# Kernel optimization log

Measured on AMD Instinct MI355X. Metric: run time of the kernel, lower is better.

## Reference

```python
import jax, jax.numpy as jnp
import numpy as np

BS, LATENT, HID, MAXLEN = 128, 512, 1024, 512

def setup_inputs() -> dict:
    key = jax.random.key(0)
    ks = jax.random.split(key, 12)
    s = 1.0 / np.sqrt(HID)  # pytorch default LSTM init scale
    inp = {}
    inp["decoder_input"] = jax.random.normal(ks[0], (BS, LATENT), jnp.float32)
    inp["lengths"] = jax.random.randint(ks[1], (BS,), 0, MAXLEN)
    # bidirectional single-layer LSTM params (gate order i,f,g,o; combined bias = b_ih+b_hh)
    inp["Wih_f"] = jax.random.uniform(ks[2], (4 * HID, LATENT), jnp.float32, -s, s)
    inp["Whh_f"] = jax.random.uniform(ks[3], (4 * HID, HID), jnp.float32, -s, s)
    inp["b_f"] = jax.random.uniform(ks[4], (4 * HID,), jnp.float32, -s, s)
    inp["Wih_b"] = jax.random.uniform(ks[5], (4 * HID, LATENT), jnp.float32, -s, s)
    inp["Whh_b"] = jax.random.uniform(ks[6], (4 * HID, HID), jnp.float32, -s, s)
    inp["b_b"] = jax.random.uniform(ks[7], (4 * HID,), jnp.float32, -s, s)
    # out: Linear(hidden -> latent); fc1: Linear(2*hidden -> 1)
    inp["W_out"] = jax.random.uniform(ks[8], (LATENT, HID), jnp.float32, -s, s)
    inp["b_out"] = jax.random.uniform(ks[9], (LATENT,), jnp.float32, -s, s)
    inp["W_fc1"] = jax.random.uniform(ks[10], (1, 2 * HID), jnp.float32, -s, s)
    inp["b_fc1"] = jax.random.uniform(ks[11], (1,), jnp.float32, -s, s)
    return inp

def _lstm_cell(x, h, c, Wih, Whh, b):
    z = x @ Wih.T + h @ Whh.T + b  # (bs, 4H)
    i, f, g, o = jnp.split(z, 4, axis=-1)
    c2 = jax.nn.sigmoid(f) * c + jax.nn.sigmoid(i) * jnp.tanh(g)
    h2 = jax.nn.sigmoid(o) * jnp.tanh(c2)
    return h2, c2

def reference(decoder_input, lengths, Wih_f, Whh_f, b_f, Wih_b, Whh_b, b_b,
              W_out, b_out, W_fc1, b_fc1):
    max_len = int(jnp.max(lengths))  # static decode length
    bs = decoder_input.shape[0]
    h0 = jnp.zeros((bs, HID), decoder_input.dtype)

    def step(carry, _):
        x, hf, cf, hb, cb = carry
        # bidirectional LSTM over a length-1 sequence = two cells on same input
        hf, cf = _lstm_cell(x, hf, cf, Wih_f, Whh_f, b_f)
        hb, cb = _lstm_cell(x, hb, cb, Wih_b, Whh_b, b_b)
        out_t = jnp.concatenate([hf, hb], axis=-1)  # (bs, 2H)
        # next input = out(h_n[-1]) i.e. backward-direction hidden
        x_next = hb @ W_out.T + b_out
        return (x_next, hf, cf, hb, cb), out_t

    carry0 = (decoder_input, h0, h0, h0, h0)
    _, outs = jax.lax.scan(step, carry0, xs=None, length=max_len)  # (T, bs, 2H)
    x = jnp.transpose(outs, (1, 0, 2))  # (bs, T, 2H)
    x = jax.nn.relu(x)
    return x @ W_fc1.T + b_fc1  # (bs, T, 1)
```

## Files before the change

kernel.cpp:

```cpp
#include <hip/hip_runtime.h>
#include <math.h>

typedef unsigned short u16;
typedef __attribute__((ext_vector_type(8))) short short8;
typedef __attribute__((ext_vector_type(4))) float f32x4;

__device__ __forceinline__ float sigm(float x) { return 1.0f / (1.0f + expf(-x)); }

__device__ __forceinline__ u16 f2bf(float x) {
    union { float f; unsigned u; } v; v.f = x;
    unsigned r = v.u + 0x7fffu + ((v.u >> 16) & 1u);
    return (u16)(r >> 16);
}
__device__ __forceinline__ float bf2f(u16 h) {
    union { unsigned u; float f; } v; v.u = ((unsigned)h) << 16;
    return v.f;
}
__device__ __forceinline__ f32x4 mfma16(short8 a, short8 b, f32x4 c) {
    return __builtin_amdgcn_mfma_f32_16x16x32_bf16(a, b, c, 0, 0, 0);
}
__device__ __forceinline__ void gl_lds16(const void* g, void* l) {
    __builtin_amdgcn_global_load_lds(
        (const __attribute__((address_space(1))) unsigned int*)g,
        (__attribute__((address_space(3))) unsigned int*)l, 16, 0, 0);
}
__device__ __forceinline__ int swz(int c) { return (c ^ (c >> 2)) & 3; }

#define FENCE() asm volatile("" ::: "memory")

#define STAGE_W(kk, buf)                                                      \
    do {                                                                      \
        gl_lds16(Wsrc + sA + (kk), sm + (buf) * 8192 + lds0);                 \
        gl_lds16(Wsrc + sB + (kk), sm + (buf) * 8192 + lds1);                 \
    } while (0)

#define LOAD_A(kk, AH_, AL_)                                                  \
    do {                                                                      \
        _Pragma("unroll") for (int ks_ = 0; ks_ < 2; ++ks_) {                 \
            AH_[ks_] = *(const short8*)(Ah + aoff + (kk) + ks_ * 32);         \
            AL_[ks_] = *(const short8*)(Al + aoff + (kk) + ks_ * 32);         \
        }                                                                     \
    } while (0)

#define COMPUTE(bix, AH_, AL_, cix)                                           \
    do {                                                                      \
        const char* bb_ = sm + (bix) * 8192;                                  \
        _Pragma("unroll") for (int ks_ = 0; ks_ < 2; ++ks_) {                 \
            short8 bh_[2], bl_[2];                                            \
            _Pragma("unroll") for (int nt_ = 0; nt_ < 2; ++nt_) {             \
                const int col_ = nt_ * 16 + l15;                              \
                const int off_ = ks_ * 2048 + col_ * 64 + ((quad ^ swz(col_)) * 16); \
                bh_[nt_] = *(const short8*)(bb_ + off_);                      \
                bl_[nt_] = *(const short8*)(bb_ + 4096 + off_);               \
            }                                                                 \
            _Pragma("unroll") for (int nt_ = 0; nt_ < 2; ++nt_) {             \
                acc[nt_] = mfma16(AH_[ks_], bh_[nt_], acc[nt_]);              \
                acc[nt_] = mfma16(AL_[ks_], bh_[nt_], acc[nt_]);              \
                acc[nt_] = mfma16(AH_[ks_], bl_[nt_], acc[nt_]);              \
            }                                                                 \
        }                                                                     \
        if (fc1w) {                                                           \
            const int kb_ = koff + (cix) * 64 + quad * 8;                     \
            _Pragma("unroll") for (int ks_ = 0; ks_ < 2; ++ks_) {             \
                const float* wp_ = smWf + kb_ + ks_ * 32;                     \
                const f32x4 w0_ = *(const f32x4*)(wp_);                       \
                const f32x4 w1_ = *(const f32x4*)(wp_ + 4);                   \
                const short8 hv_ = AH_[ks_];                                  \
                const short8 lv_ = AL_[ks_];                                  \
                _Pragma("unroll") for (int e_ = 0; e_ < 8; ++e_) {            \
                    const float v_ = bf2f((u16)hv_[e_]) + bf2f((u16)lv_[e_]); \
                    const float wv_ = (e_ < 4) ? w0_[e_] : w1_[e_ - 4];       \
                    fsum = fmaf(fmaxf(v_, 0.0f), wv_, fsum);                  \
                }                                                             \
            }                                                                 \
        }                                                                     \
    } while (0)

#define ITER(cc, BC, BS, AHU, ALU, AHL, ALL)                                  \
    do {                                                                      \
        asm volatile("s_waitcnt vmcnt(16)" ::: "memory");                     \
        __builtin_amdgcn_s_barrier();                                         \
        FENCE();                                                              \
        STAGE_W(((cc) + 3) * 64, BS);                                         \
        FENCE();                                                              \
        LOAD_A(((cc) + 3) * 64, AHL, ALL);                                    \
        COMPUTE(BC, AHU, ALU, (cc));                                          \
    } while (0)

__global__ __launch_bounds__(256, 2) void k_step(
    const u16* __restrict__ Ah, const u16* __restrict__ Al,
    u16* __restrict__ NAh, u16* __restrict__ NAl,
    const u16* __restrict__ WH, const u16* __restrict__ WL, int wstride,
    int koff_f, int nch_f, int koff_b, int nch_b,
    const float* __restrict__ BR, float* __restrict__ CF, float* __restrict__ CB,
    const float* __restrict__ Wfc1, const float* __restrict__ bfc1,
    float* __restrict__ out, int T, int t)
{
    __shared__ __align__(16) char sm[32768];
    __shared__ __align__(16) char ze[9216];
    __shared__ __align__(16) float smWf[2048];

    const int tid = threadIdx.x, bid = blockIdx.x;
    const int w = tid >> 6, lane = tid & 63, l15 = lane & 15, quad = lane >> 4;
    const int dir = bid >> 8;
    const int rest = bid & 255;
    const int rowhalf = rest >> 7, colgrp = rest & 127;
    const int nbase = dir * 4096 + colgrp * 32;
    const int koff = dir ? koff_b : koff_f;
    const int nch  = dir ? nch_b : nch_f;
    const int r0 = rowhalf * 64 + w * 16;

    const bool fc1b = (dir == 1) && (colgrp == 0);
    const bool fc1w = fc1b && (t > 0);

    const int sp = w >> 1, skh = w & 1;
    const u16* Wsrc = sp ? WL : WH;
    size_t sA, sB;
    int lds0, lds1;
    {
        const int colA = 0 * 16 + (lane >> 2);
        const int colB = 1 * 16 + (lane >> 2);
        const int sa = (lane & 3) ^ swz(colA);
        const int sb = (lane & 3) ^ swz(colB);
        sA = (size_t)(nbase + colA) * wstride + (size_t)(koff + skh * 32 + sa * 8);
        sB = (size_t)(nbase + colB) * wstride + (size_t)(koff + skh * 32 + sb * 8);
        lds0 = sp * 4096 + skh * 2048;
        lds1 = lds0 + 1024;
    }

    const size_t aoff = (size_t)(r0 + l15) * 2048 + (size_t)(koff + quad * 8);

    f32x4 acc[2] = {};
    short8 ah0[2], al0[2], ah1[2], al1[2];
    short8 ah2[2], al2[2], ah3[2], al3[2];
    float fsum = 0.0f;

    if (fc1b) {
        const f32x4 w0 = *(const f32x4*)(Wfc1 + tid * 8);
        const f32x4 w1 = *(const f32x4*)(Wfc1 + tid * 8 + 4);
        *(f32x4*)(smWf + tid * 8) = w0;
        *(f32x4*)(smWf + tid * 8 + 4) = w1;
    }
    asm volatile("s_waitcnt vmcnt(0) lgkmcnt(0)" ::: "memory");

    STAGE_W(0, 0);   FENCE(); LOAD_A(0, ah0, al0);   FENCE();
    STAGE_W(64, 1);  FENCE(); LOAD_A(64, ah1, al1);  FENCE();
    STAGE_W(128, 2); FENCE(); LOAD_A(128, ah2, al2); FENCE();

    for (int c = 0; c < nch; c += 4) {
        ITER(c + 0, 0, 3, ah0, al0, ah3, al3);
        ITER(c + 1, 1, 0, ah1, al1, ah0, al0);
        ITER(c + 2, 2, 1, ah2, al2, ah1, al1);
        ITER(c + 3, 3, 2, ah3, al3, ah2, al2);
    }
    asm volatile("s_waitcnt vmcnt(0)" ::: "memory");

    if (fc1w) {
        const size_t af = (size_t)(r0 + l15) * 2048 + (size_t)(quad * 8);
        for (int c2 = 0; c2 < 16; ++c2) {
#pragma unroll
            for (int ks = 0; ks < 2; ++ks) {
                const int ko = c2 * 64 + ks * 32;
                const short8 hv = *(const short8*)(Ah + af + ko);
                const short8 lv = *(const short8*)(Al + af + ko);
                const float* wp = smWf + ko + quad * 8;
                const f32x4 w0 = *(const f32x4*)(wp);
                const f32x4 w1 = *(const f32x4*)(wp + 4);
#pragma unroll
                for (int e = 0; e < 8; ++e) {
                    const float v = bf2f((u16)hv[e]) + bf2f((u16)lv[e]);
                    const float wv = (e < 4) ? w0[e] : w1[e - 4];
                    fsum = fmaf(fmaxf(v, 0.0f), wv, fsum);
                }
            }
        }
        float v = fsum;
        v += __shfl_xor(v, 16);
        v += __shfl_xor(v, 32);
        if (lane < 16)
            out[(size_t)(r0 + l15) * T + (t - 1)] = v + bfc1[0];
    }

    char* zb = ze + w * 2304;
#pragma unroll
    for (int nt = 0; nt < 2; ++nt)
#pragma unroll
        for (int r = 0; r < 4; ++r)
            *(float*)(zb + (quad * 4 + r) * 144 + (nt * 16 + l15) * 4) = acc[nt][r];

    float* C = dir ? CB : CF;
    const int ul = lane & 7;
#pragma unroll
    for (int p2 = 0; p2 < 2; ++p2) {
        const int ml = p2 * 8 + (lane >> 3);
        const f32x4 z = *(const f32x4*)(zb + ml * 144 + ul * 16);
        const f32x4 b4 = *(const f32x4*)(BR + nbase + ul * 4);
        const float zi = z[0] + b4[0], zf = z[1] + b4[1];
        const float zg = z[2] + b4[2], zo = z[3] + b4[3];
        const int u = colgrp * 8 + ul;
        const int m = r0 + ml;
        const size_t cidx = (size_t)m * 1024 + u;
        const float cold = C[cidx];
        const float c2 = sigm(zf) * cold + sigm(zi) * tanhf(zg);
        const float h2 = sigm(zo) * tanhf(c2);
        C[cidx] = c2;
        const size_t hidx = (size_t)m * 2048 + dir * 1024 + u;
        const u16 hh = f2bf(h2);
        NAh[hidx] = hh;
        NAl[hidx] = f2bf(h2 - bf2f(hh));
    }
}

__global__ __launch_bounds__(256) void k_tail(
    const u16* __restrict__ Ah, const u16* __restrict__ Al,
    const float* __restrict__ Wfc1, const float* __restrict__ bfc1,
    float* __restrict__ out, int T)
{
    __shared__ float red[256];
    const int m = blockIdx.x, tid = threadIdx.x;
    const size_t base = (size_t)m * 2048 + tid * 8;
    const short8 hv = *(const short8*)(Ah + base);
    const short8 lv = *(const short8*)(Al + base);
    float s = 0.0f;
#pragma unroll
    for (int e = 0; e < 8; ++e) {
        const float v = bf2f((u16)hv[e]) + bf2f((u16)lv[e]);
        s = fmaf(fmaxf(v, 0.0f), Wfc1[tid * 8 + e], s);
    }
    red[tid] = s;
    __syncthreads();
    for (int off = 128; off > 0; off >>= 1) {
        if (tid < off) red[tid] += red[tid + off];
        __syncthreads();
    }
    if (tid == 0) out[(size_t)m * T + T - 1] = red[0] + bfc1[0];
}

__global__ __launch_bounds__(256, 1) void k_fold(
    const u16* __restrict__ AH, const u16* __restrict__ AL,
    const u16* __restrict__ BH, const u16* __restrict__ BL,
    const float* __restrict__ Whh_b,
    u16* __restrict__ WH, u16* __restrict__ WL)
{
    const int tid = threadIdx.x, bid = blockIdx.x;
    const int w = tid >> 6, lane = tid & 63, l15 = lane & 15, quad = lane >> 4;
    const int bm = bid >> 4, bn = bid & 15;
    const int ar0 = bm * 64 + (w & 1) * 32;
    const int br0 = bn * 64 + (w >> 1) * 32;
    f32x4 acc[2][2] = {};
    for (int k0 = 0; k0 < 512; k0 += 32) {
        short8 a_h[2], a_l[2], b_h[2], b_l[2];
#pragma unroll
        for (int mt = 0; mt < 2; ++mt) {
            const size_t o = (size_t)(ar0 + mt * 16 + l15) * 512 + k0 + quad * 8;
            a_h[mt] = *(const short8*)(AH + o);
            a_l[mt] = *(const short8*)(AL + o);
        }
#pragma unroll
        for (int nt = 0; nt < 2; ++nt) {
            const size_t o = (size_t)(br0 + nt * 16 + l15) * 512 + k0 + quad * 8;
            b_h[nt] = *(const short8*)(BH + o);
            b_l[nt] = *(const short8*)(BL + o);
        }
#pragma unroll
        for (int mt = 0; mt < 2; ++mt)
#pragma unroll
            for (int nt = 0; nt < 2; ++nt) {
                acc[mt][nt] = mfma16(a_h[mt], b_h[nt], acc[mt][nt]);
                acc[mt][nt] = mfma16(a_l[mt], b_h[nt], acc[mt][nt]);
                acc[mt][nt] = mfma16(a_h[mt], b_l[nt], acc[mt][nt]);
            }
    }
#pragma unroll
    for (int mt = 0; mt < 2; ++mt)
#pragma unroll
        for (int nt = 0; nt < 2; ++nt)
#pragma unroll
            for (int r = 0; r < 4; ++r) {
                const int row = ar0 + mt * 16 + quad * 4 + r;
                const int j = br0 + nt * 16 + l15;
                float v = acc[mt][nt][r];
                if (row >= 4096)
                    v += Whh_b[(size_t)((row & 3) * 1024 + ((row & 4095) >> 2)) * 1024 + j];
                const size_t d = (size_t)row * 2048 + 1024 + j;
                const u16 hh = f2bf(v);
                WH[d] = hh;
                WL[d] = f2bf(v - bf2f(hh));
            }
}

__global__ __launch_bounds__(256) void k_prep(
    const float* __restrict__ dec,
    const float* __restrict__ Wih_f, const float* __restrict__ Whh_f,
    const float* __restrict__ b_f, const float* __restrict__ Wih_b,
    const float* __restrict__ b_b, const float* __restrict__ W_out,
    const float* __restrict__ b_out, const float* __restrict__ b_fc1,
    u16* __restrict__ WihH, u16* __restrict__ WihL,
    u16* __restrict__ WoTH, u16* __restrict__ WoTL,
    float* __restrict__ BR0, float* __restrict__ BR1,
    u16* __restrict__ A0h, u16* __restrict__ A0l,
    u16* __restrict__ WH, u16* __restrict__ WL,
    float* __restrict__ out, int out_size)
{
    const int t = blockIdx.x * 256 + threadIdx.x;
    if (t < 524288) {
        const int colp = t >> 6, kb = (t & 63) * 8;
        const int dir = colp >> 12, u = (colp & 4095) >> 2, g = colp & 3;
        const float* src = (dir ? Wih_b : Wih_f) + (size_t)(g * 1024 + u) * 512 + kb;
        const size_t d = (size_t)colp * 512 + kb;
#pragma unroll
        for (int j = 0; j < 8; ++j) {
            const float v = src[j];
            const u16 hh = f2bf(v);
            WihH[d + j] = hh; WihL[d + j] = f2bf(v - bf2f(hh));
        }
    } else if (t < 589824) {
        const int i = t - 524288, jc = i >> 6, lb = (i & 63) * 8;
#pragma unroll
        for (int jj = 0; jj < 8; ++jj) {
            const float v = W_out[(size_t)(lb + jj) * 1024 + jc];
            const size_t d = (size_t)jc * 512 + lb + jj;
            const u16 hh = f2bf(v);
            WoTH[d] = hh; WoTL[d] = f2bf(v - bf2f(hh));
        }
    } else if (t < 598016) {
        const int colp = t - 589824;
        const int dir = colp >> 12, u = (colp & 4095) >> 2, g = colp & 3;
        const float* Wih = dir ? Wih_b : Wih_f;
        const float s = (dir ? b_b : b_f)[g * 1024 + u];
        BR0[colp] = s;
        float dot = 0.0f;
        for (int l = 0; l < 512; ++l)
            dot += Wih[(size_t)(g * 1024 + u) * 512 + l] * b_out[l];
        BR1[colp] = s + dot;
    } else if (t < 606208) {
        const int i = t - 598016, m = i >> 6, kb = (i & 63) * 8;
#pragma unroll
        for (int j = 0; j < 8; ++j) {
            const float v = dec[(size_t)m * 512 + kb + j];
            const size_t d = (size_t)m * 2048 + kb + j;
            const u16 hh = f2bf(v);
            A0h[d] = hh; A0l[d] = f2bf(v - bf2f(hh));
        }
    } else if (t < 614400) {
        const int base = (t - 606208) * 8;
        const float b0 = b_fc1[0];
#pragma unroll
        for (int j = 0; j < 8; ++j)
            if (base + j < out_size) out[base + j] = b0;
    } else {
        const int i = t - 614400, colp = i >> 7, kb = (i & 127) * 8;
        const int u = colp >> 2, g = colp & 3;
        const float* src = Whh_f + (size_t)(g * 1024 + u) * 1024 + kb;
        const size_t d = (size_t)colp * 2048 + kb;
#pragma unroll
        for (int j = 0; j < 8; ++j) {
            const float v = src[j];
            const u16 hh = f2bf(v);
            WH[d + j] = hh; WL[d + j] = f2bf(v - bf2f(hh));
        }
    }
}

extern "C" void kernel_launch(void* const* d_in, const int* in_sizes, int n_in,
                              void* d_out, int out_size, void* d_ws, size_t ws_size,
                              hipStream_t stream) {
    const float* dec   = (const float*)d_in[0];
    const float* Wih_f = (const float*)d_in[2];
    const float* Whh_f = (const float*)d_in[3];
    const float* b_f   = (const float*)d_in[4];
    const float* Wih_b = (const float*)d_in[5];
    const float* Whh_b = (const float*)d_in[6];
    const float* b_b   = (const float*)d_in[7];
    const float* W_out = (const float*)d_in[8];
    const float* b_out = (const float*)d_in[9];
    const float* W_fc1 = (const float*)d_in[10];
    const float* b_fc1 = (const float*)d_in[11];
    float* out = (float*)d_out;

    char* ws = (char*)d_ws;
    u16* WH    = (u16*)(ws);
    u16* WL    = (u16*)(ws + 33554432);
    u16* WihH  = (u16*)(ws + 67108864);
    u16* WihL  = (u16*)(ws + 75497472);
    u16* WoTH  = (u16*)(ws + 83886080);
    u16* WoTL  = (u16*)(ws + 84934656);
    u16* A0h   = (u16*)(ws + 85983232);
    u16* A0l   = (u16*)(ws + 86507520);
    u16* A1h   = (u16*)(ws + 87031808);
    u16* A1l   = (u16*)(ws + 87556096);
    float* CF  = (float*)(ws + 88080384);
    float* CB  = (float*)(ws + 88604672);
    float* BR0 = (float*)(ws + 89128960);
    float* BR1 = (float*)(ws + 89161728);

    k_prep<<<4448, 256, 0, stream>>>(dec, Wih_f, Whh_f, b_f, Wih_b, b_b,
                                     W_out, b_out, b_fc1,
                                     WihH, WihL, WoTH, WoTL, BR0, BR1,
                                     A0h, A0l, WH, WL, out, out_size);
    k_fold<<<2048, 256, 0, stream>>>(WihH, WihL, WoTH, WoTL, Whh_b, WH, WL);
    hipMemsetAsync(CF, 0, 1048576, stream);

    const int T = out_size / 128;
    u16* Abh[2] = {A0h, A1h};
    u16* Abl[2] = {A0l, A1l};
    for (int t = 0; t < T; ++t) {
        const int in = t & 1, nx = in ^ 1;
        if (t == 0) {
            k_step<<<512, 256, 0, stream>>>(A0h, A0l, A1h, A1l,
                                            WihH, WihL, 512, 0, 8, 0, 8,
                                            BR0, CF, CB, W_fc1, b_fc1, out, T, 0);
        } else {
            k_step<<<512, 256, 0, stream>>>(Abh[in], Abl[in], Abh[nx], Abl[nx],
                                            WH, WL, 2048, 0, 32, 1024, 16,
                                            BR1, CF, CB, W_fc1, b_fc1, out, T, t);
        }
    }
    k_tail<<<128, 256, 0, stream>>>(Abh[T & 1], Abl[T & 1], W_fc1, b_fc1, out, T);
}
```

Before: 18.79 ms.

## Give each wave private weight staging to remove per-chunk block barriers

Each wave now stages its own 16-column slice of the bf16 hi/lo weights into a private LDS region and computes a 32-row by 16-column tile, replacing the 16-row by 32-column tile built from weights staged cooperatively by all four waves. Because no wave reads another wave's staged data, the per-chunk s_barrier is removed and the wait threshold is raised to match the doubled number of in-flight loads. The cost is twice the LDS footprint (64KB staging, which may limit occupancy under launch_bounds 2), more A-operand loads per wave, and a clamped prefetch index at the end of the loop. The fc1 accumulation and gate epilogue are remapped to the new tiling.

```diff
diff --git a/kernel.cpp b/kernel.cpp
--- a/kernel.cpp
+++ b/kernel.cpp
@@ -30,47 +30,50 @@
 
 #define STAGE_W(kk, buf)                                                      \
     do {                                                                      \
-        gl_lds16(Wsrc + sA + (kk), sm + (buf) * 8192 + lds0);                 \
-        gl_lds16(Wsrc + sB + (kk), sm + (buf) * 8192 + lds1);                 \
+        char* d_ = sm + (buf) * 16384 + w * 4096;                             \
+        gl_lds16(WHs + sW + (kk),      d_);                                   \
+        gl_lds16(WHs + sW + (kk) + 32, d_ + 1024);                            \
+        gl_lds16(WLs + sW + (kk),      d_ + 2048);                            \
+        gl_lds16(WLs + sW + (kk) + 32, d_ + 3072);                            \
     } while (0)
 
 #define LOAD_A(kk, AH_, AL_)                                                  \
     do {                                                                      \
-        _Pragma("unroll") for (int ks_ = 0; ks_ < 2; ++ks_) {                 \
-            AH_[ks_] = *(const short8*)(Ah + aoff + (kk) + ks_ * 32);         \
-            AL_[ks_] = *(const short8*)(Al + aoff + (kk) + ks_ * 32);         \
-        }                                                                     \
+        AH_[0] = *(const short8*)(Ah + aoff0 + (kk));                         \
+        AH_[1] = *(const short8*)(Ah + aoff0 + (kk) + 32);                    \
+        AH_[2] = *(const short8*)(Ah + aoff1 + (kk));                         \
+        AH_[3] = *(const short8*)(Ah + aoff1 + (kk) + 32);                    \
+        AL_[0] = *(const short8*)(Al + aoff0 + (kk));                         \
+        AL_[1] = *(const short8*)(Al + aoff0 + (kk) + 32);                    \
+        AL_[2] = *(const short8*)(Al + aoff1 + (kk));                         \
+        AL_[3] = *(const short8*)(Al + aoff1 + (kk) + 32);                    \
     } while (0)
 
 #define COMPUTE(bix, AH_, AL_, cix)                                           \
     do {                                                                      \
-        const char* bb_ = sm + (bix) * 8192;                                  \
+        const char* bb_ = sm + (bix) * 16384 + w * 4096;                      \
         _Pragma("unroll") for (int ks_ = 0; ks_ < 2; ++ks_) {                 \
-            short8 bh_[2], bl_[2];                                            \
-            _Pragma("unroll") for (int nt_ = 0; nt_ < 2; ++nt_) {             \
-                const int col_ = nt_ * 16 + l15;                              \
-                const int off_ = ks_ * 2048 + col_ * 64 + ((quad ^ swz(col_)) * 16); \
-                bh_[nt_] = *(const short8*)(bb_ + off_);                      \
-                bl_[nt_] = *(const short8*)(bb_ + 4096 + off_);               \
-            }                                                                 \
-            _Pragma("unroll") for (int nt_ = 0; nt_ < 2; ++nt_) {             \
-                acc[nt_] = mfma16(AH_[ks_], bh_[nt_], acc[nt_]);              \
-                acc[nt_] = mfma16(AL_[ks_], bh_[nt_], acc[nt_]);              \
-                acc[nt_] = mfma16(AH_[ks_], bl_[nt_], acc[nt_]);              \
-            }                                                                 \
+            const int off_ = ks_ * 1024 + l15 * 64 + ((quad ^ swz(l15)) * 16);\
+            const short8 bh_ = *(const short8*)(bb_ + off_);                  \
+            const short8 bl_ = *(const short8*)(bb_ + 2048 + off_);           \
+            acc[0] = mfma16(AH_[ks_], bh_, acc[0]);                           \
+            acc[0] = mfma16(AL_[ks_], bh_, acc[0]);                           \
+            acc[0] = mfma16(AH_[ks_], bl_, acc[0]);                           \
+            acc[1] = mfma16(AH_[2 + ks_], bh_, acc[1]);                       \
+            acc[1] = mfma16(AL_[2 + ks_], bh_, acc[1]);                       \
+            acc[1] = mfma16(AH_[2 + ks_], bl_, acc[1]);                       \
         }                                                                     \
         if (fc1w) {                                                           \
-            const int kb_ = koff + (cix) * 64 + quad * 8;                     \
             _Pragma("unroll") for (int ks_ = 0; ks_ < 2; ++ks_) {             \
-                const float* wp_ = smWf + kb_ + ks_ * 32;                     \
+                const float* wp_ = smWf + koff + (cix) * 64 + ks_ * 32 + quad * 8; \
                 const f32x4 w0_ = *(const f32x4*)(wp_);                       \
                 const f32x4 w1_ = *(const f32x4*)(wp_ + 4);                   \
-                const short8 hv_ = AH_[ks_];                                  \
-                const short8 lv_ = AL_[ks_];                                  \
                 _Pragma("unroll") for (int e_ = 0; e_ < 8; ++e_) {            \
-                    const float v_ = bf2f((u16)hv_[e_]) + bf2f((u16)lv_[e_]); \
                     const float wv_ = (e_ < 4) ? w0_[e_] : w1_[e_ - 4];       \
-                    fsum = fmaf(fmaxf(v_, 0.0f), wv_, fsum);                  \
+                    const float v0_ = bf2f((u16)AH_[ks_][e_]) + bf2f((u16)AL_[ks_][e_]); \
+                    fsum0 = fmaf(fmaxf(v0_, 0.0f), wv_, fsum0);               \
+                    const float v1_ = bf2f((u16)AH_[2 + ks_][e_]) + bf2f((u16)AL_[2 + ks_][e_]); \
+                    fsum1 = fmaf(fmaxf(v1_, 0.0f), wv_, fsum1);               \
                 }                                                             \
             }                                                                 \
         }                                                                     \
@@ -78,12 +81,12 @@
 
 #define ITER(cc, BC, BS, AHU, ALU, AHL, ALL)                                  \
     do {                                                                      \
-        asm volatile("s_waitcnt vmcnt(16)" ::: "memory");                     \
-        __builtin_amdgcn_s_barrier();                                         \
+        asm volatile("s_waitcnt vmcnt(32)" ::: "memory");                     \
         FENCE();                                                              \
-        STAGE_W(((cc) + 3) * 64, BS);                                         \
+        const int pf_ = ((cc) + 3 < nch ? (cc) + 3 : nch - 1) * 64;           \
+        STAGE_W(pf_, BS);                                                     \
         FENCE();                                                              \
-        LOAD_A(((cc) + 3) * 64, AHL, ALL);                                    \
+        LOAD_A(pf_, AHL, ALL);                                                \
         COMPUTE(BC, AHU, ALU, (cc));                                          \
     } while (0)
 
@@ -96,8 +99,7 @@
     const float* __restrict__ Wfc1, const float* __restrict__ bfc1,
     float* __restrict__ out, int T, int t)
 {
-    __shared__ __align__(16) char sm[32768];
-    __shared__ __align__(16) char ze[9216];
+    __shared__ __align__(16) char sm[65536];
     __shared__ __align__(16) float smWf[2048];
 
     const int tid = threadIdx.x, bid = blockIdx.x;
@@ -108,32 +110,28 @@
     const int nbase = dir * 4096 + colgrp * 32;
     const int koff = dir ? koff_b : koff_f;
     const int nch  = dir ? nch_b : nch_f;
-    const int r0 = rowhalf * 64 + w * 16;
+    const int rg = w >> 1, ch = w & 1;
+    const int r0w = rowhalf * 64 + rg * 32;
 
     const bool fc1b = (dir == 1) && (colgrp == 0);
-    const bool fc1w = fc1b && (t > 0);
-
-    const int sp = w >> 1, skh = w & 1;
-    const u16* Wsrc = sp ? WL : WH;
-    size_t sA, sB;
-    int lds0, lds1;
+    const bool fc1w = fc1b && (t > 0) && (ch == 0);
+
+    const u16* WHs = WH;
+    const u16* WLs = WL;
+    size_t sW;
     {
-        const int colA = 0 * 16 + (lane >> 2);
-        const int colB = 1 * 16 + (lane >> 2);
-        const int sa = (lane & 3) ^ swz(colA);
-        const int sb = (lane & 3) ^ swz(colB);
-        sA = (size_t)(nbase + colA) * wstride + (size_t)(koff + skh * 32 + sa * 8);
-        sB = (size_t)(nbase + colB) * wstride + (size_t)(koff + skh * 32 + sb * 8);
-        lds0 = sp * 4096 + skh * 2048;
-        lds1 = lds0 + 1024;
-    }
-
-    const size_t aoff = (size_t)(r0 + l15) * 2048 + (size_t)(koff + quad * 8);
+        const int col = lane >> 2;
+        const int s = (lane & 3) ^ swz(col);
+        sW = (size_t)(nbase + ch * 16 + col) * wstride + (size_t)(koff + s * 8);
+    }
+
+    const size_t aoff0 = (size_t)(r0w + l15) * 2048 + (size_t)(koff + quad * 8);
+    const size_t aoff1 = aoff0 + (size_t)16 * 2048;
 
     f32x4 acc[2] = {};
-    short8 ah0[2], al0[2], ah1[2], al1[2];
-    short8 ah2[2], al2[2], ah3[2], al3[2];
-    float fsum = 0.0f;
+    short8 ah0[4], al0[4], ah1[4], al1[4];
+    short8 ah2[4], al2[4], ah3[4], al3[4];
+    float fsum0 = 0.0f, fsum1 = 0.0f;
 
     if (fc1b) {
         const f32x4 w0 = *(const f32x4*)(Wfc1 + tid * 8);
@@ -142,6 +140,7 @@
         *(f32x4*)(smWf + tid * 8 + 4) = w1;
     }
     asm volatile("s_waitcnt vmcnt(0) lgkmcnt(0)" ::: "memory");
+    __builtin_amdgcn_s_barrier();
 
     STAGE_W(0, 0);   FENCE(); LOAD_A(0, ah0, al0);   FENCE();
     STAGE_W(64, 1);  FENCE(); LOAD_A(64, ah1, al1);  FENCE();
@@ -156,49 +155,61 @@
     asm volatile("s_waitcnt vmcnt(0)" ::: "memory");
 
     if (fc1w) {
-        const size_t af = (size_t)(r0 + l15) * 2048 + (size_t)(quad * 8);
         for (int c2 = 0; c2 < 16; ++c2) {
 #pragma unroll
             for (int ks = 0; ks < 2; ++ks) {
                 const int ko = c2 * 64 + ks * 32;
-                const short8 hv = *(const short8*)(Ah + af + ko);
-                const short8 lv = *(const short8*)(Al + af + ko);
+                const size_t a0 = (size_t)(r0w + l15) * 2048 + quad * 8 + ko;
+                const size_t a1 = a0 + (size_t)16 * 2048;
+                const short8 hv0 = *(const short8*)(Ah + a0);
+                const short8 lv0 = *(const short8*)(Al + a0);
+                const short8 hv1 = *(const short8*)(Ah + a1);
+                const short8 lv1 = *(const short8*)(Al + a1);
                 const float* wp = smWf + ko + quad * 8;
                 const f32x4 w0 = *(const f32x4*)(wp);
                 const f32x4 w1 = *(const f32x4*)(wp + 4);
 #pragma unroll
                 for (int e = 0; e < 8; ++e) {
-                    const float v = bf2f((u16)hv[e]) + bf2f((u16)lv[e]);
                     const float wv = (e < 4) ? w0[e] : w1[e - 4];
-                    fsum = fmaf(fmaxf(v, 0.0f), wv, fsum);
+                    const float v0 = bf2f((u16)hv0[e]) + bf2f((u16)lv0[e]);
+                    fsum0 = fmaf(fmaxf(v0, 0.0f), wv, fsum0);
+                    const float v1 = bf2f((u16)hv1[e]) + bf2f((u16)lv1[e]);
+                    fsum1 = fmaf(fmaxf(v1, 0.0f), wv, fsum1);
                 }
             }
         }
-        float v = fsum;
-        v += __shfl_xor(v, 16);
-        v += __shfl_xor(v, 32);
-        if (lane < 16)
-            out[(size_t)(r0 + l15) * T + (t - 1)] = v + bfc1[0];
-    }
-
-    char* zb = ze + w * 2304;
-#pragma unroll
-    for (int nt = 0; nt < 2; ++nt)
+        float v0 = fsum0;
+        v0 += __shfl_xor(v0, 16);
+        v0 += __shfl_xor(v0, 32);
+        float v1 = fsum1;
+        v1 += __shfl_xor(v1, 16);
+        v1 += __shfl_xor(v1, 32);
+        if (lane < 16) {
+            out[(size_t)(r0w + l15) * T + (t - 1)] = v0 + bfc1[0];
+            out[(size_t)(r0w + 16 + l15) * T + (t - 1)] = v1 + bfc1[0];
+        }
+    }
+
+    char* zb = sm + w * 4096;
+#pragma unroll
+    for (int rt = 0; rt < 2; ++rt)
 #pragma unroll
         for (int r = 0; r < 4; ++r)
-            *(float*)(zb + (quad * 4 + r) * 144 + (nt * 16 + l15) * 4) = acc[nt][r];
+            *(float*)(zb + (rt * 16 + quad * 4 + r) * 80 + l15 * 4) =
+                (rt ? acc[1][r] : acc[0][r]);
 
     float* C = dir ? CB : CF;
-    const int ul = lane & 7;
 #pragma unroll
     for (int p2 = 0; p2 < 2; ++p2) {
-        const int ml = p2 * 8 + (lane >> 3);
-        const f32x4 z = *(const f32x4*)(zb + ml * 144 + ul * 16);
-        const f32x4 b4 = *(const f32x4*)(BR + nbase + ul * 4);
+        const int idx = p2 * 64 + lane;
+        const int ml = idx >> 2;
+        const int ul = idx & 3;
+        const f32x4 z = *(const f32x4*)(zb + ml * 80 + ul * 16);
+        const f32x4 b4 = *(const f32x4*)(BR + nbase + ch * 16 + ul * 4);
         const float zi = z[0] + b4[0], zf = z[1] + b4[1];
         const float zg = z[2] + b4[2], zo = z[3] + b4[3];
-        const int u = colgrp * 8 + ul;
-        const int m = r0 + ml;
+        const int u = colgrp * 8 + ch * 4 + ul;
+        const int m = r0w + ml;
         const size_t cidx = (size_t)m * 1024 + u;
         const float cold = C[cidx];
         const float c2 = sigm(zf) * cold + sigm(zi) * tanhf(zg);
```

New measurement: 34.43 ms. 83.2% more time.
